# Optimization experiments

Measured on AMD Instinct MI355X. Metric: run time of the kernel, lower is better.

Reference implementation:

```python
import jax, jax.numpy as jnp
import numpy as np

B = 4096        # number of sets
MAX_N = 64      # max set size (matches max(n) in data)
DIM = 256       # per-element feature dim
W = 32          # weight_dim = sqrt(hidden_dim=1024)


def sinusoid_pe(length, dim):
    # standard transformer sinusoid PE: pe[p,2i]=sin(p/10000^(2i/dim)), pe[p,2i+1]=cos(...)
    pos = jnp.arange(length, dtype=jnp.float32)[:, None]
    i = jnp.arange(dim)[None, :]
    angle = pos / jnp.power(10000.0, (2.0 * (i // 2)).astype(jnp.float32) / dim)
    return jnp.where(i % 2 == 0, jnp.sin(angle), jnp.cos(angle))


def setup_inputs() -> dict:
    key = jax.random.key(0)
    ks = jax.random.split(key, 6)
    # ragged batch: alternating set sizes 32 and 64, 2048 each -> 196608 rows
    counts = np.tile(np.array([32, 64], dtype=np.int64), B // 2)
    batch = jnp.asarray(np.repeat(np.arange(B, dtype=np.int64), counts))
    N = int(counts.sum())
    x = jax.random.normal(ks[0], (N, DIM), dtype=jnp.float32)
    s = 1.0 / np.sqrt(DIM)
    Wk = jax.random.normal(ks[1], (W, DIM), dtype=jnp.float32) * s
    Wv = jax.random.normal(ks[2], (W, DIM), dtype=jnp.float32) * s
    Wq = jax.random.normal(ks[3], (W, DIM), dtype=jnp.float32) * s
    Wmap = jax.random.normal(ks[4], (DIM, W), dtype=jnp.float32) / np.sqrt(W)
    bmap = jax.random.normal(ks[5], (DIM,), dtype=jnp.float32) * 0.01
    return {"x": x, "batch": batch, "Wk": Wk, "Wv": Wv, "Wq": Wq, "Wmap": Wmap, "bmap": bmap}


def reference(x, batch, Wk, Wv, Wq, Wmap, bmap):
    N = x.shape[0]
    # set sizes and within-set positions (vectorized replacement of torch python loops)
    n = jax.ops.segment_sum(jnp.ones((N,), jnp.int32), batch, num_segments=B)
    ptr = jnp.concatenate([jnp.zeros((1,), jnp.int32), jnp.cumsum(n)])[:-1]
    pos_in_set = jnp.arange(N, dtype=jnp.int32) - ptr[batch]

    # --- Encoder ---
    xmat = jnp.zeros((B, MAX_N, DIM), x.dtype).at[batch, pos_in_set].set(x)
    mask = jnp.zeros((B, MAX_N), bool).at[batch, pos_in_set].set(True)
    pe = sinusoid_pe(MAX_N, DIM)                       # [MAX_N, DIM]
    xpos = xmat + pe[None]                             # [B, MAX_N, DIM]
    m = mask[..., None].astype(x.dtype)
    yk = jnp.einsum('bnd,wd->bnw', xpos, Wk) * m       # [B, MAX_N, W]
    yv = jnp.einsum('bnd,wd->bnw', xpos, Wv) * m
    # z_mat[b,i,j] = sum_n yv[b,n,i] * yk[b,n,j]
    z_mat = jnp.einsum('bnj,bni->bij', yk, yv)         # [B, W, W]

    # --- Decoder ---
    query = sinusoid_pe(MAX_N, DIM) @ Wq.T             # [MAX_N, W]
    decoded = jnp.einsum('mk,bkv->bmv', query, z_mat)  # [B, MAX_N, W]
    x_padded = decoded @ Wmap.T + bmap                 # [B, MAX_N, DIM]
    # unpad: gather valid rows back to flat ragged layout
    x_out = x_padded[batch, pos_in_set]                # [N, DIM]
    return (x_out, batch)
```

## Files before the change

### kernel.cpp

```cpp
#include <hip/hip_runtime.h>
#include <math.h>

#define N_SETS 4096
#define SETS_PER_BLOCK 4
#define GRID_MAIN (N_SETS / SETS_PER_BLOCK)

typedef _Float16 f16;
typedef __attribute__((ext_vector_type(8))) _Float16 f16x8;
typedef __attribute__((ext_vector_type(4))) _Float16 f16x4;
typedef __attribute__((ext_vector_type(4))) float     f32x4;

#define WS_PE    0
#define WS_QH    65536
#define WS_WKV   69632
#define WS_WMAPH 102400
#define WS_PEH   118784
#define WS_PTR   151552

__global__ void k_aux1(const int* __restrict__ batch, float* __restrict__ out2,
                       int* __restrict__ ptr, int N, float* __restrict__ pe) {
    int blk = blockIdx.x;
    if (blk < 768) {
        int i = blk * 256 + threadIdx.x;
        if (i >= N) return;
        int b = batch[i];
        out2[i] = (float)b;
        if (i == 0 || batch[i - 1] != b) ptr[b] = i;
        if (i == N - 1) ptr[N_SETS] = N;
    } else {
        int idx = (blk - 768) * 256 + threadIdx.x;
        int p = idx >> 8, i = idx & 255;
        float e   = (float)(2 * (i / 2)) / 256.0f;
        float inv = powf(10000.0f, -e);
        float ang = (float)p * inv;
        pe[idx] = (i & 1) ? cosf(ang) : sinf(ang);
    }
}

__global__ void k_aux2(const float* __restrict__ Wk, const float* __restrict__ Wv,
                       const float* __restrict__ Wq, const float* __restrict__ Wmap,
                       const float* __restrict__ pe, f16* __restrict__ wkv,
                       f16* __restrict__ wmaph, f16* __restrict__ peh,
                       f16* __restrict__ qh) {
    int blk = blockIdx.x;
    if (blk < 96) {
        int idx = blk * 256 + threadIdx.x;
        if (idx < 16384) {
            int j = idx >> 8, d = idx & 255;
            float v = (j < 32) ? Wk[j * 256 + d] : Wv[(j - 32) * 256 + d];
            wkv[idx] = (f16)v;
        } else {
            int i2 = idx - 16384;
            wmaph[i2] = (f16)Wmap[i2];
        }
    } else if (blk < 160) {
        int idx = (blk - 96) * 256 + threadIdx.x;
        peh[idx] = (f16)pe[idx];
    } else {
        int idx = (blk - 160) * 256 + threadIdx.x;
        int pos = idx >> 5, k = idx & 31;
        const float* pr = pe + pos * 256;
        const float* wr = Wq + k * 256;
        float s = 0.f;
        for (int d = 0; d < 256; d += 4) {
            float4 a = *(const float4*)(pr + d);
            float4 b = *(const float4*)(wr + d);
            s += a.x * b.x + a.y * b.y + a.z * b.z + a.w * b.w;
        }
        qh[idx] = (f16)s;
    }
}

__global__ __launch_bounds__(256, 2) void k_main(
        const float* __restrict__ x,     const f16* __restrict__ wkv,
        const f16* __restrict__ wmaph,   const f16* __restrict__ qh,
        const f16* __restrict__ peh,     const float* __restrict__ bmap,
        const int* __restrict__ ptr,     float* __restrict__ out) {
    __shared__ char lds[43008];
    char* ysh = lds + 32768;
    char* dsh = lds + 32768;
    char* zsh = lds + 40960;

    const int t    = threadIdx.x;
    const int wv   = t >> 6;
    const int l15  = t & 15;
    const int lhi  = (t & 63) >> 4;
    const int arow = 16 * wv + l15;
    const int swz7 = (l15 & 7) << 4;

    int pv[SETS_PER_BLOCK + 1];
    #pragma unroll
    for (int i = 0; i <= SETS_PER_BLOCK; ++i)
        pv[i] = ptr[blockIdx.x * SETS_PER_BLOCK + i];

    #pragma unroll
    for (int i2 = 0; i2 < 8; ++i2) {
        int c = t + 256 * i2;
        int j = c >> 5, d0 = (c & 31) * 8;
        *(f16x8*)(lds + ((j * 512 + d0 * 2) ^ ((j & 7) << 4))) =
            *(const f16x8*)(wkv + j * 256 + d0);
    }
    f16x8 pef[8];
    #pragma unroll
    for (int ks = 0; ks < 8; ++ks)
        pef[ks] = *(const f16x8*)(peh + arow * 256 + ks * 32 + lhi * 8);
    const f16x8 qreg = *(const f16x8*)(qh + arow * 32 + lhi * 8);
    f16x8 bwreg[4];
    float bm[4];
    #pragma unroll
    for (int i = 0; i < 4; ++i) {
        const int dcol = 64 * wv + 16 * i + l15;
        bwreg[i] = *(const f16x8*)(wmaph + dcol * 32 + lhi * 8);
        bm[i] = bmap[dcol];
    }

    float4 xf[8];
    {
        const int s0 = pv[0], n0 = pv[1] - pv[0];
        if (arow < n0) {
            const float* xr = x + (size_t)(s0 + arow) * 256 + lhi * 8;
            #pragma unroll
            for (int ks = 0; ks < 4; ++ks) {
                xf[2 * ks]     = *(const float4*)(xr + ks * 32);
                xf[2 * ks + 1] = *(const float4*)(xr + ks * 32 + 4);
            }
        }
    }
    __syncthreads();

    for (int j = 0; j < SETS_PER_BLOCK; ++j) {
        const int s = pv[j], n = pv[j + 1] - s;
        const int n32 = (n + 31) & ~31;
        const float* xr = x + (size_t)(s + arow) * 256 + lhi * 8;

        f16x8 areg[8];
        if (arow < n) {
            #pragma unroll
            for (int ks = 0; ks < 4; ++ks) {
                float4 a = xf[2 * ks], a2 = xf[2 * ks + 1];
                f16x8 h;
                h[0]=(f16)a.x;  h[1]=(f16)a.y;  h[2]=(f16)a.z;  h[3]=(f16)a.w;
                h[4]=(f16)a2.x; h[5]=(f16)a2.y; h[6]=(f16)a2.z; h[7]=(f16)a2.w;
                areg[ks] = h + pef[ks];
            }
            #pragma unroll
            for (int ks = 4; ks < 8; ++ks) {
                float4 a  = *(const float4*)(xr + ks * 32);
                float4 a2 = *(const float4*)(xr + ks * 32 + 4);
                f16x8 h;
                h[0]=(f16)a.x;  h[1]=(f16)a.y;  h[2]=(f16)a.z;  h[3]=(f16)a.w;
                h[4]=(f16)a2.x; h[5]=(f16)a2.y; h[6]=(f16)a2.z; h[7]=(f16)a2.w;
                areg[ks] = h + pef[ks];
            }
        } else {
            #pragma unroll
            for (int ks = 0; ks < 8; ++ks) {
                f16x8 h;
                #pragma unroll
                for (int ii = 0; ii < 8; ++ii) h[ii] = (f16)0.f;
                areg[ks] = h;
            }
        }
        if (j + 1 < SETS_PER_BLOCK) {
            const int s1 = pv[j + 1], n1 = pv[j + 2] - pv[j + 1];
            if (arow < n1) {
                const float* xr1 = x + (size_t)(s1 + arow) * 256 + lhi * 8;
                #pragma unroll
                for (int ks = 0; ks < 4; ++ks) {
                    xf[2 * ks]     = *(const float4*)(xr1 + ks * 32);
                    xf[2 * ks + 1] = *(const float4*)(xr1 + ks * 32 + 4);
                }
            }
        }

        if (16 * wv < n32) {
            f32x4 acc[4];
            #pragma unroll
            for (int nt = 0; nt < 4; ++nt) acc[nt] = (f32x4){0.f, 0.f, 0.f, 0.f};
            #pragma unroll
            for (int ks = 0; ks < 8; ++ks) {
                #pragma unroll
                for (int nt = 0; nt < 4; ++nt) {
                    f16x8 bf = *(const f16x8*)(lds +
                        (((16 * nt + l15) * 512 + ks * 64 + lhi * 16) ^ swz7));
                    acc[nt] = __builtin_amdgcn_mfma_f32_16x16x32_f16(areg[ks], bf, acc[nt], 0, 0, 0);
                }
            }
            const int row0 = 16 * wv + lhi * 4;
            #pragma unroll
            for (int nt = 0; nt < 4; ++nt) {
                const int col = 16 * nt + l15;
                f16x4 h4;
                #pragma unroll
                for (int q = 0; q < 4; ++q) h4[q] = (f16)acc[nt][q];
                *(f16x4*)(ysh + ((col * 128 + row0 * 2) ^ swz7)) = h4;
            }
        }
        __syncthreads();

        {
            const int it = wv >> 1, jt = wv & 1;
            f32x4 zacc = {0.f, 0.f, 0.f, 0.f};
            const int ca = 32 + 16 * it + l15, cb = 16 * jt + l15;
            const int nks = n32 >> 5;
            for (int ks = 0; ks < nks; ++ks) {
                const int r2 = ks * 64 + lhi * 16;
                f16x8 av = *(const f16x8*)(ysh + ((ca * 128 + r2) ^ swz7));
                f16x8 bk = *(const f16x8*)(ysh + ((cb * 128 + r2) ^ swz7));
                zacc = __builtin_amdgcn_mfma_f32_16x16x32_f16(av, bk, zacc, 0, 0, 0);
            }
            const int zc = 16 * jt + l15, zr0 = 16 * it + lhi * 4;
            f16x4 h4;
            #pragma unroll
            for (int q = 0; q < 4; ++q) h4[q] = (f16)zacc[q];
            *(f16x4*)(zsh + ((zc * 64 + zr0 * 2) ^ ((l15 & 3) << 4))) = h4;
        }
        __syncthreads();

        if (16 * wv < n) {
            const int k2 = lhi * 16;
            f16x8 bz0 = *(const f16x8*)(zsh + ((l15 * 64 + k2) ^ ((l15 & 3) << 4)));
            f16x8 bz1 = *(const f16x8*)(zsh + (((16 + l15) * 64 + k2) ^ ((l15 & 3) << 4)));
            f32x4 dd0 = {0.f, 0.f, 0.f, 0.f}, dd1 = {0.f, 0.f, 0.f, 0.f};
            dd0 = __builtin_amdgcn_mfma_f32_16x16x32_f16(qreg, bz0, dd0, 0, 0, 0);
            dd1 = __builtin_amdgcn_mfma_f32_16x16x32_f16(qreg, bz1, dd1, 0, 0, 0);
            #pragma unroll
            for (int q = 0; q < 4; ++q) {
                const int m = 16 * wv + lhi * 4 + q;
                *(f16*)(dsh + ((m * 64 + l15 * 2) ^ ((m & 7) << 4)))        = (f16)dd0[q];
                *(f16*)(dsh + ((m * 64 + (16 + l15) * 2) ^ ((m & 7) << 4))) = (f16)dd1[q];
            }
        }
        __syncthreads();

        {
            const int k2 = lhi * 16;
            float* ob = out + (size_t)s * 256;
            #pragma unroll
            for (int mt = 0; mt < 4; ++mt) {
                if (16 * mt < n) {
                    f16x8 ad = *(const f16x8*)(dsh + (((16 * mt + l15) * 64 + k2) ^ swz7));
                    const int row0 = 16 * mt + lhi * 4;
                    #pragma unroll
                    for (int i = 0; i < 4; ++i) {
                        const int dcol = 64 * wv + 16 * i + l15;
                        f32x4 o = {0.f, 0.f, 0.f, 0.f};
                        o = __builtin_amdgcn_mfma_f32_16x16x32_f16(ad, bwreg[i], o, 0, 0, 0);
                        #pragma unroll
                        for (int q = 0; q < 4; ++q) {
                            const int row = row0 + q;
                            if (row < n) ob[(size_t)row * 256 + dcol] = o[q] + bm[i];
                        }
                    }
                }
            }
        }
        __syncthreads();
    }
}

extern "C" void kernel_launch(void* const* d_in, const int* in_sizes, int n_in,
                              void* d_out, int out_size, void* d_ws, size_t ws_size,
                              hipStream_t stream) {
    const float* x    = (const float*)d_in[0];
    const int*   batch= (const int*)  d_in[1];
    const float* Wk   = (const float*)d_in[2];
    const float* Wv   = (const float*)d_in[3];
    const float* Wq   = (const float*)d_in[4];
    const float* Wmap = (const float*)d_in[5];
    const float* bmap = (const float*)d_in[6];
    float* out = (float*)d_out;

    const int N = in_sizes[1];
    float* pe    = (float*)((char*)d_ws + WS_PE);
    f16*   qh    = (f16*)  ((char*)d_ws + WS_QH);
    f16*   wkv   = (f16*)  ((char*)d_ws + WS_WKV);
    f16*   wmaph = (f16*)  ((char*)d_ws + WS_WMAPH);
    f16*   peh   = (f16*)  ((char*)d_ws + WS_PEH);
    int*   ptr   = (int*)  ((char*)d_ws + WS_PTR);
    float* out2  = out + (size_t)N * 256;

    k_aux1<<<832, 256, 0, stream>>>(batch, out2, ptr, N, pe);
    k_aux2<<<168, 256, 0, stream>>>(Wk, Wv, Wq, Wmap, pe, wkv, wmaph, peh, qh);
    k_main<<<GRID_MAIN, 256, 0, stream>>>(x, wkv, wmaph, qh, peh, bmap, ptr, out);
}
```

Measured before the change: 115.4 us.

## Vectorize output stores, prefetch full x rows, and double sets per block

The output GEMM is transposed with the bias preloaded into the MFMA accumulator, so each lane writes a contiguous f32x4 instead of scattered scalar stores, and the per-row bounds check is dropped. The whole next-set x row is now prefetched into registers, and each block handles 8 sets instead of 4. The decoded buffer gets its own LDS region, which removes the trailing barrier. The remaining barriers become a raw lgkmcnt wait plus s_barrier. The trade-off is more registers and LDS, which may hurt occupancy, and unmasked stores that assume set sizes are multiples of 16.

```diff
diff --git a/kernel.cpp b/kernel.cpp
--- a/kernel.cpp
+++ b/kernel.cpp
@@ -2,7 +2,7 @@
 #include <math.h>
 
 #define N_SETS 4096
-#define SETS_PER_BLOCK 4
+#define SETS_PER_BLOCK 8
 #define GRID_MAIN (N_SETS / SETS_PER_BLOCK)
 
 typedef _Float16 f16;
@@ -16,6 +16,12 @@
 #define WS_WMAPH 102400
 #define WS_PEH   118784
 #define WS_PTR   151552
+
+__device__ __forceinline__ void lds_barrier() {
+    asm volatile("s_waitcnt lgkmcnt(0)" ::: "memory");
+    __builtin_amdgcn_s_barrier();
+    __builtin_amdgcn_sched_barrier(0);
+}
 
 __global__ void k_aux1(const int* __restrict__ batch, float* __restrict__ out2,
                        int* __restrict__ ptr, int N, float* __restrict__ pe) {
@@ -76,10 +82,10 @@
         const f16* __restrict__ wmaph,   const f16* __restrict__ qh,
         const f16* __restrict__ peh,     const float* __restrict__ bmap,
         const int* __restrict__ ptr,     float* __restrict__ out) {
-    __shared__ char lds[43008];
+    __shared__ char lds[47104];
     char* ysh = lds + 32768;
-    char* dsh = lds + 32768;
     char* zsh = lds + 40960;
+    char* dsh = lds + 43008;
 
     const int t    = threadIdx.x;
     const int wv   = t >> 6;
@@ -106,52 +112,42 @@
         pef[ks] = *(const f16x8*)(peh + arow * 256 + ks * 32 + lhi * 8);
     const f16x8 qreg = *(const f16x8*)(qh + arow * 32 + lhi * 8);
     f16x8 bwreg[4];
-    float bm[4];
+    f32x4 biasc[4];
     #pragma unroll
     for (int i = 0; i < 4; ++i) {
-        const int dcol = 64 * wv + 16 * i + l15;
-        bwreg[i] = *(const f16x8*)(wmaph + dcol * 32 + lhi * 8);
-        bm[i] = bmap[dcol];
-    }
-
-    float4 xf[8];
+        const int dcol = 64 * wv + 16 * i;
+        bwreg[i] = *(const f16x8*)(wmaph + (dcol + l15) * 32 + lhi * 8);
+        biasc[i] = *(const f32x4*)(bmap + dcol + lhi * 4);
+    }
+
+    float4 xf[16];
     {
         const int s0 = pv[0], n0 = pv[1] - pv[0];
         if (arow < n0) {
             const float* xr = x + (size_t)(s0 + arow) * 256 + lhi * 8;
             #pragma unroll
-            for (int ks = 0; ks < 4; ++ks) {
+            for (int ks = 0; ks < 8; ++ks) {
                 xf[2 * ks]     = *(const float4*)(xr + ks * 32);
                 xf[2 * ks + 1] = *(const float4*)(xr + ks * 32 + 4);
             }
         }
     }
-    __syncthreads();
+    lds_barrier();
 
     for (int j = 0; j < SETS_PER_BLOCK; ++j) {
         const int s = pv[j], n = pv[j + 1] - s;
         const int n32 = (n + 31) & ~31;
-        const float* xr = x + (size_t)(s + arow) * 256 + lhi * 8;
 
         f16x8 areg[8];
         if (arow < n) {
             #pragma unroll
-            for (int ks = 0; ks < 4; ++ks) {
+            for (int ks = 0; ks < 8; ++ks) {
                 float4 a = xf[2 * ks], a2 = xf[2 * ks + 1];
                 f16x8 h;
                 h[0]=(f16)a.x;  h[1]=(f16)a.y;  h[2]=(f16)a.z;  h[3]=(f16)a.w;
                 h[4]=(f16)a2.x; h[5]=(f16)a2.y; h[6]=(f16)a2.z; h[7]=(f16)a2.w;
                 areg[ks] = h + pef[ks];
             }
-            #pragma unroll
-            for (int ks = 4; ks < 8; ++ks) {
-                float4 a  = *(const float4*)(xr + ks * 32);
-                float4 a2 = *(const float4*)(xr + ks * 32 + 4);
-                f16x8 h;
-                h[0]=(f16)a.x;  h[1]=(f16)a.y;  h[2]=(f16)a.z;  h[3]=(f16)a.w;
-                h[4]=(f16)a2.x; h[5]=(f16)a2.y; h[6]=(f16)a2.z; h[7]=(f16)a2.w;
-                areg[ks] = h + pef[ks];
-            }
         } else {
             #pragma unroll
             for (int ks = 0; ks < 8; ++ks) {
@@ -166,7 +162,7 @@
             if (arow < n1) {
                 const float* xr1 = x + (size_t)(s1 + arow) * 256 + lhi * 8;
                 #pragma unroll
-                for (int ks = 0; ks < 4; ++ks) {
+                for (int ks = 0; ks < 8; ++ks) {
                     xf[2 * ks]     = *(const float4*)(xr1 + ks * 32);
                     xf[2 * ks + 1] = *(const float4*)(xr1 + ks * 32 + 4);
                 }
@@ -196,7 +192,7 @@
                 *(f16x4*)(ysh + ((col * 128 + row0 * 2) ^ swz7)) = h4;
             }
         }
-        __syncthreads();
+        lds_barrier();
 
         {
             const int it = wv >> 1, jt = wv & 1;
@@ -215,7 +211,7 @@
             for (int q = 0; q < 4; ++q) h4[q] = (f16)zacc[q];
             *(f16x4*)(zsh + ((zc * 64 + zr0 * 2) ^ ((l15 & 3) << 4))) = h4;
         }
-        __syncthreads();
+        lds_barrier();
 
         if (16 * wv < n) {
             const int k2 = lhi * 16;
@@ -231,7 +227,7 @@
                 *(f16*)(dsh + ((m * 64 + (16 + l15) * 2) ^ ((m & 7) << 4))) = (f16)dd1[q];
             }
         }
-        __syncthreads();
+        lds_barrier();
 
         {
             const int k2 = lhi * 16;
@@ -240,22 +236,14 @@
             for (int mt = 0; mt < 4; ++mt) {
                 if (16 * mt < n) {
                     f16x8 ad = *(const f16x8*)(dsh + (((16 * mt + l15) * 64 + k2) ^ swz7));
-                    const int row0 = 16 * mt + lhi * 4;
                     #pragma unroll
                     for (int i = 0; i < 4; ++i) {
-                        const int dcol = 64 * wv + 16 * i + l15;
-                        f32x4 o = {0.f, 0.f, 0.f, 0.f};
-                        o = __builtin_amdgcn_mfma_f32_16x16x32_f16(ad, bwreg[i], o, 0, 0, 0);
-                        #pragma unroll
-                        for (int q = 0; q < 4; ++q) {
-                            const int row = row0 + q;
-                            if (row < n) ob[(size_t)row * 256 + dcol] = o[q] + bm[i];
-                        }
+                        f32x4 o = __builtin_amdgcn_mfma_f32_16x16x32_f16(bwreg[i], ad, biasc[i], 0, 0, 0);
+                        *(f32x4*)(ob + (size_t)(16 * mt + l15) * 256 + 64 * wv + 16 * i + lhi * 4) = o;
                     }
                 }
             }
         }
-        __syncthreads();
     }
 }
 
```

Result: faster. 111.6 us (-3.4%).
